# Kernel tuning notes

Hardware: AMD Instinct MI355X
Metric: run time of the kernel (lower is better)

Reference implementation:

```python
import jax, jax.numpy as jnp
import numpy as np


def setup_inputs() -> dict:
    key = jax.random.key(0)
    ks = jax.random.split(key, 4)
    B, S, D, U = 4, 4096, 128, 64
    x = jax.random.normal(ks[0], (B, S, D), dtype=jnp.float32)
    Wq = jax.random.normal(ks[1], (D, U), dtype=jnp.float32) * (1.0 / np.sqrt(D))
    Wk = jax.random.normal(ks[2], (D, U), dtype=jnp.float32) * (1.0 / np.sqrt(D))
    Wv = jax.random.normal(ks[3], (D, U), dtype=jnp.float32) * (1.0 / np.sqrt(D))
    bq = jnp.zeros((U,), dtype=jnp.float32)
    bk = jnp.zeros((U,), dtype=jnp.float32)
    bv = jnp.zeros((U,), dtype=jnp.float32)
    return {"x": x, "Wq": Wq, "bq": bq, "Wk": Wk, "bk": bk, "Wv": Wv, "bv": bv}


def reference(x, Wq, bq, Wk, bk, Wv, bv):
    # Single-head, unscaled, unmasked attention (faithful to the Keras layer).
    q = jnp.einsum("bsd,du->bsu", x, Wq) + bq  # [B,S,U]
    k = jnp.einsum("bsd,du->bsu", x, Wk) + bk  # [B,S,U]
    v = jnp.einsum("bsd,du->bsu", x, Wv) + bv  # [B,S,U]
    scores = jnp.einsum("bsu,btu->bst", q, k)  # [B,S,S], no 1/sqrt(d) scaling
    attn = jax.nn.softmax(scores, axis=-1)
    return jnp.einsum("bst,btu->bsu", attn, v)  # [B,S,U]
```

## Files before the change

### kernel.cpp

```cpp
#include <hip/hip_runtime.h>
#include <hip/hip_fp16.h>
#include <math.h>

#define SEQ   4096
#define DIM   128
#define UDIM  64
#define BATCH 4
#define BS    (BATCH*SEQ)
#define NT    (SEQ/64)
#define NSPLIT 6

typedef _Float16 h8 __attribute__((ext_vector_type(8)));
typedef _Float16 h4 __attribute__((ext_vector_type(4)));
typedef _Float16 h2 __attribute__((ext_vector_type(2)));
typedef float    f4 __attribute__((ext_vector_type(4)));

#define MFMA_K32(a,b,c) __builtin_amdgcn_mfma_f32_16x16x32_f16((a),(b),(c),0,0,0)
#define MFMA_K16(a,b,c) __builtin_amdgcn_mfma_f32_16x16x16f16((a),(b),(c),0,0,0)

__device__ __forceinline__ h2 pk2(float a, float b) {
  return __builtin_bit_cast(h2, __builtin_amdgcn_cvt_pkrtz(a, b));
}
__device__ __forceinline__ float fexp2(float x) {
#if __has_builtin(__builtin_amdgcn_exp2f)
  return __builtin_amdgcn_exp2f(x);
#else
  return exp2f(x);
#endif
}

#define WT_STRIDE 272
#define KB_STRIDE 144
#define L2E 1.44269504088896f


__global__ __launch_bounds__(256, 2) void proj_mfma(
    const float* __restrict__ x,
    const float* __restrict__ Wq, const float* __restrict__ bq,
    const float* __restrict__ Wk, const float* __restrict__ bk,
    const float* __restrict__ Wv, const float* __restrict__ bv,
    _Float16* __restrict__ qf, _Float16* __restrict__ kswz, _Float16* __restrict__ vswz)
{
  const int tid  = threadIdx.x;
  const int lane = tid & 63, wv = tid >> 6;
  const int n = lane & 15, quad = lane >> 4;
  const int r0 = blockIdx.x * 64;

  __shared__ __align__(16) char wlds[3][UDIM * WT_STRIDE];
  __shared__ __align__(16) char kbnc[4 * 16 * KB_STRIDE];

  #pragma unroll
  for (int p = 0; p < 3; ++p) {
    const float* __restrict__ W = (p == 0) ? Wq : ((p == 1) ? Wk : Wv);
    #pragma unroll
    for (int i = 0; i < 8; ++i) {
      const int idx = i*256 + tid;
      const int nn  = idx & 63;
      const int k4  = (idx >> 6) * 4;
      const float w0 = W[(k4+0)*UDIM + nn];
      const float w1 = W[(k4+1)*UDIM + nn];
      const float w2 = W[(k4+2)*UDIM + nn];
      const float w3 = W[(k4+3)*UDIM + nn];
      int2 wd;
      wd.x = __builtin_bit_cast(int, pk2(w0, w1));
      wd.y = __builtin_bit_cast(int, pk2(w2, w3));
      *(int2*)(wlds[p] + nn*WT_STRIDE + k4*2) = wd;
    }
  }

  const int row = r0 + wv*16 + n;
  h8 xa[4];
  #pragma unroll
  for (int ks = 0; ks < 4; ++ks) {
    const float* xp = x + (size_t)row*DIM + ks*32 + quad*8;
    const f4 a = *(const f4*)xp, b = *(const f4*)(xp + 4);
    int4 pkd;
    pkd.x = __builtin_bit_cast(int, pk2(a[0], a[1]));
    pkd.y = __builtin_bit_cast(int, pk2(a[2], a[3]));
    pkd.z = __builtin_bit_cast(int, pk2(b[0], b[1]));
    pkd.w = __builtin_bit_cast(int, pk2(b[2], b[3]));
    xa[ks] = __builtin_bit_cast(h8, pkd);
  }
  __syncthreads();

  const int b  = r0 / SEQ;
  const int kb = ((r0 % SEQ) >> 4) + wv;

  #pragma unroll
  for (int p = 0; p < 3; ++p) {
    const float* __restrict__ bias = (p == 0) ? bq : ((p == 1) ? bk : bv);
    f4 acc[4];
    #pragma unroll
    for (int nt = 0; nt < 4; ++nt) acc[nt] = (f4){0.f,0.f,0.f,0.f};
    #pragma unroll
    for (int ks = 0; ks < 4; ++ks)
      #pragma unroll
      for (int nt = 0; nt < 4; ++nt) {
        const h8 wf = *(const h8*)(wlds[p] + (nt*16 + n)*WT_STRIDE + (ks*32 + quad*8)*2);
        acc[nt] = MFMA_K32(xa[ks], wf, acc[nt]);
      }
    #pragma unroll
    for (int nt = 0; nt < 4; ++nt) {
      const float bb = bias[nt*16 + n];
      #pragma unroll
      for (int r = 0; r < 4; ++r) acc[nt][r] += bb;
    }

    if (p == 0) {
      #pragma unroll
      for (int nt = 0; nt < 4; ++nt)
        #pragma unroll
        for (int r = 0; r < 4; ++r) acc[nt][r] *= L2E;
      const int par = lane & 1;
      const unsigned sel = par ? 0x03020706u : 0x05040100u;
      #pragma unroll
      for (int nt = 0; nt < 4; ++nt)
        #pragma unroll
        for (int pp = 0; pp < 2; ++pp) {
          const int r = 2*pp;
          unsigned A  = __builtin_bit_cast(unsigned, pk2(acc[nt][r], acc[nt][r+1]));
          unsigned Bs = (unsigned)__builtin_amdgcn_mov_dpp((int)A, 0xB1, 0xF, 0xF, true);
          unsigned w  = __builtin_amdgcn_perm(Bs, A, sel);
          const int orow = r0 + wv*16 + 4*quad + r + par;
          const int ocol = nt*16 + n - par;
          *(unsigned*)((char*)qf + ((size_t)orow*UDIM + ocol)*2) = w;
        }
    } else if (p == 1) {
      char* base = kbnc + wv*(16*KB_STRIDE);
      #pragma unroll
      for (int nt = 0; nt < 4; ++nt)
        #pragma unroll
        for (int r = 0; r < 4; ++r)
          *(_Float16*)(base + (4*quad + r)*KB_STRIDE + (nt*16 + n)*2) =
              (_Float16)acc[nt][r];
      _Float16* kdst = kswz + (size_t)b*SEQ*UDIM;
      #pragma unroll
      for (int ks = 0; ks < 2; ++ks) {
        const h8 f = *(const h8*)(base + n*KB_STRIDE + ks*64 + quad*16);
        *(h8*)(kdst + ((size_t)(kb*2 + ks)*64 + lane)*8) = f;
      }
    } else {
      _Float16* vdst = vswz + (size_t)b*SEQ*UDIM;
      #pragma unroll
      for (int pr = 0; pr < 2; ++pr) {
        int4 t;
        t.x = __builtin_bit_cast(int, pk2(acc[2*pr][0],   acc[2*pr][1]));
        t.y = __builtin_bit_cast(int, pk2(acc[2*pr][2],   acc[2*pr][3]));
        t.z = __builtin_bit_cast(int, pk2(acc[2*pr+1][0], acc[2*pr+1][1]));
        t.w = __builtin_bit_cast(int, pk2(acc[2*pr+1][2], acc[2*pr+1][3]));
        *(int4*)(vdst + ((size_t)(kb*2 + pr)*64 + lane)*8) = t;
      }
    }
  }
}

__global__ __launch_bounds__(256, 3) void flash_attn_t(
    const _Float16* __restrict__ qf, const _Float16* __restrict__ kswz,
    const _Float16* __restrict__ vswz,
    _Float16* __restrict__ opart, float* __restrict__ Mp, float* __restrict__ Lp)
{
  const int qt = blockIdx.x, b = blockIdx.y, sp = blockIdx.z;
  const int ns = gridDim.z;
  const int kt0 = (sp * NT) / ns;
  const int kt1 = ((sp + 1) * NT) / ns;
  const int tid = threadIdx.x;
  const int lane = tid & 63, wid = tid >> 6;
  const int n = lane & 15, quad = lane >> 4;
  const int qbase = qt*128 + wid*32;

  const _Float16* __restrict__ qb = qf + (size_t)b*SEQ*UDIM;
  const _Float16* kpl = kswz + (size_t)b*SEQ*UDIM + (size_t)kt0*4096 + lane*8;
  const _Float16* kph = kpl + 2048;
  const _Float16* vpl = vswz + (size_t)b*SEQ*UDIM + (size_t)kt0*4096 + lane*8;
  const _Float16* vph = vpl + 2048;

  h8 qB[2][2];
  #pragma unroll
  for (int nt = 0; nt < 2; ++nt)
    #pragma unroll
    for (int ks = 0; ks < 2; ++ks)
      qB[nt][ks] = *(const h8*)(qb + (size_t)(qbase + nt*16 + n)*UDIM + ks*32 + quad*8);

  f4 O[4][2], Ol[2];
  #pragma unroll
  for (int ut = 0; ut < 4; ++ut)
    #pragma unroll
    for (int nt = 0; nt < 2; ++nt) O[ut][nt] = (f4){0.f,0.f,0.f,0.f};
  Ol[0] = (f4){0.f,0.f,0.f,0.f};
  Ol[1] = (f4){0.f,0.f,0.f,0.f};

  float M[2] = {-1e30f, -1e30f};

  h4 ones_a;
  { const _Float16 o = (_Float16)1.0f;
    ones_a[0]=o; ones_a[1]=o; ones_a[2]=o; ones_a[3]=o; }

  h8 ka[4][2];
  ka[0][0] = *(const h8*)(kpl);        ka[0][1] = *(const h8*)(kpl +  512);
  ka[1][0] = *(const h8*)(kpl + 1024); ka[1][1] = *(const h8*)(kpl + 1536);
  ka[2][0] = *(const h8*)(kph);        ka[2][1] = *(const h8*)(kph +  512);
  ka[3][0] = *(const h8*)(kph + 1024); ka[3][1] = *(const h8*)(kph + 1536);

  for (int t = kt0; t < kt1; ++t) {
    h8 va8[8];
    va8[0] = *(const h8*)(vpl);        va8[1] = *(const h8*)(vpl +  512);
    va8[2] = *(const h8*)(vpl + 1024); va8[3] = *(const h8*)(vpl + 1536);
    va8[4] = *(const h8*)(vph);        va8[5] = *(const h8*)(vph +  512);
    va8[6] = *(const h8*)(vph + 1024); va8[7] = *(const h8*)(vph + 1536);

    f4 S[4][2];
    #pragma unroll
    for (int mt = 0; mt < 4; ++mt)
      #pragma unroll
      for (int nt = 0; nt < 2; ++nt) S[mt][nt] = (f4){0.f,0.f,0.f,0.f};
    #pragma unroll
    for (int ks = 0; ks < 2; ++ks)
      #pragma unroll
      for (int mt = 0; mt < 4; ++mt)
        #pragma unroll
        for (int nt = 0; nt < 2; ++nt)
          S[mt][nt] = MFMA_K32(ka[mt][ks], qB[nt][ks], S[mt][nt]);

    if (t + 1 < kt1) {
      kpl += 4096; kph += 4096;
      ka[0][0] = *(const h8*)(kpl);        ka[0][1] = *(const h8*)(kpl +  512);
      ka[1][0] = *(const h8*)(kpl + 1024); ka[1][1] = *(const h8*)(kpl + 1536);
      ka[2][0] = *(const h8*)(kph);        ka[2][1] = *(const h8*)(kph +  512);
      ka[3][0] = *(const h8*)(kph + 1024); ka[3][1] = *(const h8*)(kph + 1536);
    }

    float mn[2];
    #pragma unroll
    for (int nt = 0; nt < 2; ++nt) {
      float m0 = fmaxf(fmaxf(S[0][nt][0], S[0][nt][1]), fmaxf(S[0][nt][2], S[0][nt][3]));
      float m1 = fmaxf(fmaxf(S[1][nt][0], S[1][nt][1]), fmaxf(S[1][nt][2], S[1][nt][3]));
      float m2 = fmaxf(fmaxf(S[2][nt][0], S[2][nt][1]), fmaxf(S[2][nt][2], S[2][nt][3]));
      float m3 = fmaxf(fmaxf(S[3][nt][0], S[3][nt][1]), fmaxf(S[3][nt][2], S[3][nt][3]));
      float rm = fmaxf(fmaxf(m0, m1), fmaxf(m2, m3));
      rm = fmaxf(rm, __shfl_xor(rm, 16));
      rm = fmaxf(rm, __shfl_xor(rm, 32));
      mn[nt] = fmaxf(M[nt], rm);
    }

    const bool nochange = (mn[0] == M[0]) && (mn[1] == M[1]);
    if (!__all(nochange)) {
      #pragma unroll
      for (int nt = 0; nt < 2; ++nt) {
        const float alpha = fexp2(M[nt] - mn[nt]);
        #pragma unroll
        for (int ut = 0; ut < 4; ++ut)
          #pragma unroll
          for (int r = 0; r < 4; ++r) O[ut][nt][r] *= alpha;
        #pragma unroll
        for (int r = 0; r < 4; ++r) Ol[nt][r] *= alpha;
      }
    }
    M[0] = mn[0]; M[1] = mn[1];

    h4 pB[4][2];
    #pragma unroll
    for (int mt = 0; mt < 4; ++mt)
      #pragma unroll
      for (int nt = 0; nt < 2; ++nt) {
        #pragma unroll
        for (int r = 0; r < 4; ++r)
          S[mt][nt][r] = fexp2(S[mt][nt][r] - mn[nt]);
        int2 tt;
        tt.x = __builtin_bit_cast(int, pk2(S[mt][nt][0], S[mt][nt][1]));
        tt.y = __builtin_bit_cast(int, pk2(S[mt][nt][2], S[mt][nt][3]));
        pB[mt][nt] = __builtin_bit_cast(h4, tt);
      }

    #pragma unroll
    for (int mt = 0; mt < 4; ++mt) {
      const int4 vi0 = __builtin_bit_cast(int4, va8[2*mt]);
      const int4 vi1 = __builtin_bit_cast(int4, va8[2*mt+1]);
      int2 p01, p23, p45, p67;
      p01.x = vi0.x; p01.y = vi0.y;  p23.x = vi0.z; p23.y = vi0.w;
      p45.x = vi1.x; p45.y = vi1.y;  p67.x = vi1.z; p67.y = vi1.w;
      h4 va[4];
      va[0] = __builtin_bit_cast(h4, p01);
      va[1] = __builtin_bit_cast(h4, p23);
      va[2] = __builtin_bit_cast(h4, p45);
      va[3] = __builtin_bit_cast(h4, p67);
      #pragma unroll
      for (int ut = 0; ut < 4; ++ut)
        #pragma unroll
        for (int nt = 0; nt < 2; ++nt)
          O[ut][nt] = MFMA_K16(va[ut], pB[mt][nt], O[ut][nt]);
      #pragma unroll
      for (int nt = 0; nt < 2; ++nt)
        Ol[nt] = MFMA_K16(ones_a, pB[mt][nt], Ol[nt]);
    }

    vpl += 4096; vph += 4096;
  }

  const size_t rowg = (size_t)sp*BS + (size_t)b*SEQ + qbase;
  #pragma unroll
  for (int nt = 0; nt < 2; ++nt) {
    char* __restrict__ orow = (char*)(opart + (rowg + nt*16 + n)*UDIM);
    #pragma unroll
    for (int ut = 0; ut < 4; ++ut)
      #pragma unroll
      for (int p = 0; p < 2; ++p)
        *(unsigned*)(orow + (ut*16 + quad*4 + 2*p)*2) =
            __builtin_bit_cast(unsigned, pk2(O[ut][nt][2*p], O[ut][nt][2*p+1]));
    if (quad == 0) {
      Mp[rowg + nt*16 + n] = M[nt];
      Lp[rowg + nt*16 + n] = Ol[nt][0];
    }
  }
}

__global__ __launch_bounds__(256) void merge_out(
    const _Float16* __restrict__ opart, const float* __restrict__ Mp,
    const float* __restrict__ Lp, float* __restrict__ out, int nsplit)
{
  const int tid = threadIdx.x;
  const int row = blockIdx.x*16 + (tid >> 4);
  const int u4  = (tid & 15) * 4;
  float M = -1e30f;
  for (int s = 0; s < nsplit; ++s) M = fmaxf(M, Mp[(size_t)s*BS + row]);
  f4 num = (f4){0.f,0.f,0.f,0.f};
  float den = 0.f;
  for (int s = 0; s < nsplit; ++s) {
    const float w = fexp2(Mp[(size_t)s*BS + row] - M);
    den += w * Lp[(size_t)s*BS + row];
    const h4 op = *(const h4*)(opart + ((size_t)s*BS + row)*UDIM + u4);
    #pragma unroll
    for (int i = 0; i < 4; ++i) num[i] += w * (float)op[i];
  }
  const float dinv = 1.f / den;
  *(f4*)(out + (size_t)row*UDIM + u4) = num * dinv;
}

extern "C" void kernel_launch(void* const* d_in, const int* in_sizes, int n_in,
                              void* d_out, int out_size, void* d_ws, size_t ws_size,
                              hipStream_t stream) {
  (void)in_sizes; (void)n_in; (void)out_size;
  const float* x  = (const float*)d_in[0];
  const float* Wq = (const float*)d_in[1];
  const float* bq = (const float*)d_in[2];
  const float* Wk = (const float*)d_in[3];
  const float* bk = (const float*)d_in[4];
  const float* Wv = (const float*)d_in[5];
  const float* bv = (const float*)d_in[6];
  float* out = (float*)d_out;

  char* ws = (char*)d_ws;
  const size_t fBytes = (size_t)BS * UDIM * 2;
  auto need = [](int nsp) {
    return (size_t)3*BS*UDIM*2 + (size_t)nsp*BS*4*2 + (size_t)nsp*BS*UDIM*2;
  };
  int nsplit;
  if      (ws_size >= need(NSPLIT)) nsplit = NSPLIT;
  else if (ws_size >= need(4))      nsplit = 4;
  else if (ws_size >= need(2))      nsplit = 2;
  else                              nsplit = 1;

  _Float16* qf   = (_Float16*)(ws);
  _Float16* kswz = (_Float16*)(ws + fBytes);
  _Float16* vswz = (_Float16*)(ws + 2*fBytes);
  float* Mp      = (float*)(ws + 3*fBytes);
  float* Lp      = (float*)(ws + 3*fBytes + (size_t)nsplit*BS*4);
  _Float16* opart = (_Float16*)(ws + 3*fBytes + (size_t)nsplit*BS*8);

  proj_mfma<<<dim3(BS/64), 256, 0, stream>>>(x, Wq, bq, Wk, bk, Wv, bv, qf, kswz, vswz);
  flash_attn_t<<<dim3(SEQ/128, BATCH, nsplit), 256, 0, stream>>>(
      qf, kswz, vswz, opart, Mp, Lp);
  merge_out<<<dim3(BS/16), 256, 0, stream>>>(opart, Mp, Lp, out, nsplit);
}
```

Baseline: 114.7 us.

## Use K32 MFMA for PV product via bpermute-rearranged P and new V layout

Switches the P·V and row-sum accumulation from 16x16x16 MFMAs to 16x16x32 MFMAs, halving the MFMA instruction count in that stage. To feed the wider K, the exponentiated P fragments are rearranged across lanes with ds_bpermute, and the projection kernel writes V in a matching swizzled layout. V loads are split so the second half is fetched after the first permute. The cost is sixteen extra cross-lane permute instructions per tile, with their LDS-path latency and select operations.

```diff
diff --git a/kernel.cpp b/kernel.cpp
--- a/kernel.cpp
+++ b/kernel.cpp
@@ -16,7 +16,6 @@
 typedef float    f4 __attribute__((ext_vector_type(4)));
 
 #define MFMA_K32(a,b,c) __builtin_amdgcn_mfma_f32_16x16x32_f16((a),(b),(c),0,0,0)
-#define MFMA_K16(a,b,c) __builtin_amdgcn_mfma_f32_16x16x16f16((a),(b),(c),0,0,0)
 
 __device__ __forceinline__ h2 pk2(float a, float b) {
   return __builtin_bit_cast(h2, __builtin_amdgcn_cvt_pkrtz(a, b));
@@ -85,6 +84,7 @@
 
   const int b  = r0 / SEQ;
   const int kb = ((r0 % SEQ) >> 4) + wv;
+  const int vt = (r0 % SEQ) >> 6;
 
   #pragma unroll
   for (int p = 0; p < 3; ++p) {
@@ -140,15 +140,16 @@
         *(h8*)(kdst + ((size_t)(kb*2 + ks)*64 + lane)*8) = f;
       }
     } else {
-      _Float16* vdst = vswz + (size_t)b*SEQ*UDIM;
-      #pragma unroll
-      for (int pr = 0; pr < 2; ++pr) {
-        int4 t;
-        t.x = __builtin_bit_cast(int, pk2(acc[2*pr][0],   acc[2*pr][1]));
-        t.y = __builtin_bit_cast(int, pk2(acc[2*pr][2],   acc[2*pr][3]));
-        t.z = __builtin_bit_cast(int, pk2(acc[2*pr+1][0], acc[2*pr+1][1]));
-        t.w = __builtin_bit_cast(int, pk2(acc[2*pr+1][2], acc[2*pr+1][3]));
-        *(int4*)(vdst + ((size_t)(kb*2 + pr)*64 + lane)*8) = t;
+      _Float16* vdst = vswz + (size_t)b*SEQ*UDIM + (size_t)vt*4096;
+      const int hh = wv >> 1;
+      const int qp = 2*(wv & 1) + (quad >> 1);
+      const int jb = (quad & 1) * 4;
+      #pragma unroll
+      for (int nt = 0; nt < 4; ++nt) {
+        int2 t;
+        t.x = __builtin_bit_cast(int, pk2(acc[nt][0], acc[nt][1]));
+        t.y = __builtin_bit_cast(int, pk2(acc[nt][2], acc[nt][3]));
+        *(int2*)(vdst + (hh*4 + nt)*512 + (16*qp + n)*8 + jb) = t;
       }
     }
   }
@@ -191,9 +192,14 @@
 
   float M[2] = {-1e30f, -1e30f};
 
-  h4 ones_a;
+  h8 ones8;
   { const _Float16 o = (_Float16)1.0f;
-    ones_a[0]=o; ones_a[1]=o; ones_a[2]=o; ones_a[3]=o; }
+    #pragma unroll
+    for (int i = 0; i < 8; ++i) ones8[i] = o; }
+
+  const int alo4 = ((32*((lane >> 4) & 1) + (lane & 15)) << 2);
+  const int ahi4 = alo4 + 64;
+  const bool qlo = (lane < 32);
 
   h8 ka[4][2];
   ka[0][0] = *(const h8*)(kpl);        ka[0][1] = *(const h8*)(kpl +  512);
@@ -202,11 +208,9 @@
   ka[3][0] = *(const h8*)(kph + 1024); ka[3][1] = *(const h8*)(kph + 1536);
 
   for (int t = kt0; t < kt1; ++t) {
-    h8 va8[8];
-    va8[0] = *(const h8*)(vpl);        va8[1] = *(const h8*)(vpl +  512);
-    va8[2] = *(const h8*)(vpl + 1024); va8[3] = *(const h8*)(vpl + 1536);
-    va8[4] = *(const h8*)(vph);        va8[5] = *(const h8*)(vph +  512);
-    va8[6] = *(const h8*)(vph + 1024); va8[7] = *(const h8*)(vph + 1536);
+    h8 va0[4];
+    va0[0] = *(const h8*)(vpl);        va0[1] = *(const h8*)(vpl +  512);
+    va0[2] = *(const h8*)(vpl + 1024); va0[3] = *(const h8*)(vpl + 1536);
 
     f4 S[4][2];
     #pragma unroll
@@ -271,27 +275,65 @@
         pB[mt][nt] = __builtin_bit_cast(h4, tt);
       }
 
-    #pragma unroll
-    for (int mt = 0; mt < 4; ++mt) {
-      const int4 vi0 = __builtin_bit_cast(int4, va8[2*mt]);
-      const int4 vi1 = __builtin_bit_cast(int4, va8[2*mt+1]);
-      int2 p01, p23, p45, p67;
-      p01.x = vi0.x; p01.y = vi0.y;  p23.x = vi0.z; p23.y = vi0.w;
-      p45.x = vi1.x; p45.y = vi1.y;  p67.x = vi1.z; p67.y = vi1.w;
-      h4 va[4];
-      va[0] = __builtin_bit_cast(h4, p01);
-      va[1] = __builtin_bit_cast(h4, p23);
-      va[2] = __builtin_bit_cast(h4, p45);
-      va[3] = __builtin_bit_cast(h4, p67);
-      #pragma unroll
-      for (int ut = 0; ut < 4; ++ut)
-        #pragma unroll
-        for (int nt = 0; nt < 2; ++nt)
-          O[ut][nt] = MFMA_K16(va[ut], pB[mt][nt], O[ut][nt]);
+    h8 pb32a[2];
+    #pragma unroll
+    for (int nt = 0; nt < 2; ++nt) {
+      const int2 X = __builtin_bit_cast(int2, pB[0][nt]);
+      const int2 Y = __builtin_bit_cast(int2, pB[1][nt]);
+      int4 o;
+      { int a0 = __builtin_amdgcn_ds_bpermute(alo4, X.x);
+        int b0 = __builtin_amdgcn_ds_bpermute(alo4, Y.x);
+        int a1 = __builtin_amdgcn_ds_bpermute(alo4, X.y);
+        int b1 = __builtin_amdgcn_ds_bpermute(alo4, Y.y);
+        int a2 = __builtin_amdgcn_ds_bpermute(ahi4, X.x);
+        int b2 = __builtin_amdgcn_ds_bpermute(ahi4, Y.x);
+        int a3 = __builtin_amdgcn_ds_bpermute(ahi4, X.y);
+        int b3 = __builtin_amdgcn_ds_bpermute(ahi4, Y.y);
+        o.x = qlo ? a0 : b0; o.y = qlo ? a1 : b1;
+        o.z = qlo ? a2 : b2; o.w = qlo ? a3 : b3; }
+      pb32a[nt] = __builtin_bit_cast(h8, o);
+    }
+
+    h8 va1[4];
+    va1[0] = *(const h8*)(vph);        va1[1] = *(const h8*)(vph +  512);
+    va1[2] = *(const h8*)(vph + 1024); va1[3] = *(const h8*)(vph + 1536);
+
+    #pragma unroll
+    for (int ut = 0; ut < 4; ++ut)
       #pragma unroll
       for (int nt = 0; nt < 2; ++nt)
-        Ol[nt] = MFMA_K16(ones_a, pB[mt][nt], Ol[nt]);
-    }
+        O[ut][nt] = MFMA_K32(va0[ut], pb32a[nt], O[ut][nt]);
+    #pragma unroll
+    for (int nt = 0; nt < 2; ++nt)
+      Ol[nt] = MFMA_K32(ones8, pb32a[nt], Ol[nt]);
+
+    h8 pb32b[2];
+    #pragma unroll
+    for (int nt = 0; nt < 2; ++nt) {
+      const int2 X = __builtin_bit_cast(int2, pB[2][nt]);
+      const int2 Y = __builtin_bit_cast(int2, pB[3][nt]);
+      int4 o;
+      { int a0 = __builtin_amdgcn_ds_bpermute(alo4, X.x);
+        int b0 = __builtin_amdgcn_ds_bpermute(alo4, Y.x);
+        int a1 = __builtin_amdgcn_ds_bpermute(alo4, X.y);
+        int b1 = __builtin_amdgcn_ds_bpermute(alo4, Y.y);
+        int a2 = __builtin_amdgcn_ds_bpermute(ahi4, X.x);
+        int b2 = __builtin_amdgcn_ds_bpermute(ahi4, Y.x);
+        int a3 = __builtin_amdgcn_ds_bpermute(ahi4, X.y);
+        int b3 = __builtin_amdgcn_ds_bpermute(ahi4, Y.y);
+        o.x = qlo ? a0 : b0; o.y = qlo ? a1 : b1;
+        o.z = qlo ? a2 : b2; o.w = qlo ? a3 : b3; }
+      pb32b[nt] = __builtin_bit_cast(h8, o);
+    }
+
+    #pragma unroll
+    for (int ut = 0; ut < 4; ++ut)
+      #pragma unroll
+      for (int nt = 0; nt < 2; ++nt)
+        O[ut][nt] = MFMA_K32(va1[ut], pb32b[nt], O[ut][nt]);
+    #pragma unroll
+    for (int nt = 0; nt < 2; ++nt)
+      Ol[nt] = MFMA_K32(ones8, pb32b[nt], Ol[nt]);
 
     vpl += 4096; vph += 4096;
   }
```

Measured after the change: 109.6 us (median of 2 runs). 1.05x faster.
